# Performance work log

Hardware: AMD Instinct MI355X
Metric: run time of the kernel (lower is better)

Reference implementation:

```python
import jax, jax.numpy as jnp
import numpy as np

N_DF = 96      # number of deep-filtered frequency bins
BASE = 0       # base_bin
N_ORDER = 5    # FIR taps along time


def setup_inputs() -> dict:
    key = jax.random.key(0)
    k1, k2 = jax.random.split(key)
    B, T, F = 8, 3000, 481
    # complex spectrogram stored as [..., 2] = (real, imag)
    spec = jax.random.normal(k1, (B, T, F, 2), dtype=jnp.float32)
    # per-frame complex FIR coefficients: [..., :N_ORDER]=real, [..., N_ORDER:]=imag
    coef = jax.random.normal(k2, (B, T, N_DF, 2 * N_ORDER), dtype=jnp.float32)
    return {"spec": spec, "coef": coef}


def _df_forward(spec, coef):
    T = spec.shape[1]
    # narrow to the deep-filter band
    xr = spec[:, :, BASE:BASE + N_DF, 0]  # [B,T,N_DF]
    xi = spec[:, :, BASE:BASE + N_DF, 1]
    # causal pad along time (ConstantPad2d((0,0,n_order-1,0)))
    pad = ((0, 0), (N_ORDER - 1, 0), (0, 0))
    pr = jnp.pad(xr, pad)
    pi = jnp.pad(xi, pad)
    # unfold(time, n_order, 1) -> [B,T,N_DF,N_ORDER]; loop is over fixed tap count
    ur = jnp.stack([pr[:, k:k + T] for k in range(N_ORDER)], axis=-1)
    ui = jnp.stack([pi[:, k:k + T] for k in range(N_ORDER)], axis=-1)
    cr = coef[..., :N_ORDER]
    ci = coef[..., N_ORDER:]
    # complex sliding dot product: sum_k u[k] * c[k]
    fr = jnp.sum(ur * cr - ui * ci, axis=-1)  # [B,T,N_DF]
    fi = jnp.sum(ur * ci + ui * cr, axis=-1)
    out = spec.at[:, :, BASE:BASE + N_DF, 0].set(fr)
    out = out.at[:, :, BASE:BASE + N_DF, 1].set(fi)
    return out


def reference(spec, coef):
    return _df_forward(spec, coef)
```

## Files before the change

### kernel.cpp

```cpp
#include <hip/hip_runtime.h>


#define BN   8
#define TN   3000
#define FN   481
#define NDF  96
#define NORD 5

__global__ __launch_bounds__(256) void df_kernel(const float* __restrict__ spec,
                                                 const float* __restrict__ coef,
                                                 float* __restrict__ out) {
    const int i = blockIdx.x * blockDim.x + threadIdx.x;
    const int nFilt = BN * TN * NDF;
    const int nTot  = BN * TN * FN;
    if (i >= nTot) return;

    const int rowStride = FN * 2;

    if (i < nFilt) {
        const int f  = i % NDF;
        const int bt = i / NDF;
        const int t  = bt % TN;

        const float2* c2 = (const float2*)(coef + (size_t)i * (2 * NORD));
        const float2 ca = c2[0], cb = c2[1], cc = c2[2], cd = c2[3], ce = c2[4];
        const float cr[NORD] = {ca.x, ca.y, cb.x, cb.y, cc.x};
        const float ci[NORD] = {cc.y, cd.x, cd.y, ce.x, ce.y};

        const int base0 = bt * rowStride + f * 2;

        float fr = 0.f, fi = 0.f;
        if (t >= NORD - 1) {
            #pragma unroll
            for (int k = 0; k < NORD; ++k) {
                const float2 x = *(const float2*)(spec + base0 + (k - (NORD - 1)) * rowStride);
                fr += x.x * cr[k] - x.y * ci[k];
                fi += x.x * ci[k] + x.y * cr[k];
            }
        } else {
            #pragma unroll
            for (int k = 0; k < NORD; ++k) {
                const int tt = t - (NORD - 1) + k;
                if (tt >= 0) {
                    const float2 x = *(const float2*)(spec + base0 + (k - (NORD - 1)) * rowStride);
                    fr += x.x * cr[k] - x.y * ci[k];
                    fi += x.x * ci[k] + x.y * cr[k];
                }
            }
        }
        *(float2*)(out + base0) = make_float2(fr, fi);
    } else {
        const int j  = i - nFilt;
        const int f  = NDF + j % (FN - NDF);
        const int bt = j / (FN - NDF);
        const int idx = bt * rowStride + f * 2;
        *(float2*)(out + idx) = *(const float2*)(spec + idx);
    }
}

extern "C" void kernel_launch(void* const* d_in, const int* in_sizes, int n_in,
                              void* d_out, int out_size, void* d_ws, size_t ws_size,
                              hipStream_t stream) {
    const float* spec = (const float*)d_in[0];
    const float* coef = (const float*)d_in[1];
    float* out = (float*)d_out;

    const int nTot = BN * TN * FN;
    const int block = 256;
    const int grid = (nTot + block - 1) / block;
    df_kernel<<<grid, block, 0, stream>>>(spec, coef, out);
}
```

Before: 226.4 us.

## Stage coefficients via coalesced LDS loads and vectorize passthrough copy with float4

Filter blocks now load their contiguous 10-float coefficient slab with coalesced float4 loads into shared memory, replacing strided per-thread float2 reads. The copy region handles row alignment parity so most of each row moves as float4, plus one float2 per row, cutting the number of memory instructions and threads. The costs are added shared-memory traffic, a block barrier, and some index arithmetic.

```diff
diff --git a/kernel.cpp b/kernel.cpp
--- a/kernel.cpp
+++ b/kernel.cpp
@@ -6,55 +6,72 @@
 #define FN   481
 #define NDF  96
 #define NORD 5
+#define ROWF (FN * 2)
+#define NROWS (BN * TN)
+#define NFILT (NROWS * NDF)
+#define FILT_BLOCKS (NFILT / 256)
+#define COPYU 193
+#define NCOPY (NROWS * COPYU)
+#define COPY_BLOCKS ((NCOPY + 255) / 256)
 
-__global__ __launch_bounds__(256) void df_kernel(const float* __restrict__ spec,
-                                                 const float* __restrict__ coef,
-                                                 float* __restrict__ out) {
-    const int i = blockIdx.x * blockDim.x + threadIdx.x;
-    const int nFilt = BN * TN * NDF;
-    const int nTot  = BN * TN * FN;
-    if (i >= nTot) return;
+__global__ __launch_bounds__(256) void df_fused(const float* __restrict__ spec,
+                                                const float* __restrict__ coef,
+                                                float* __restrict__ out) {
+    const int blk = blockIdx.x;
+    const int tid = threadIdx.x;
 
-    const int rowStride = FN * 2;
+    if (blk < FILT_BLOCKS) {
+        __shared__ __align__(16) float cbuf[256 * 10];
+        {
+            const float4* src = (const float4*)(coef + (size_t)blk * 2560);
+            float4* dst = (float4*)cbuf;
+            dst[tid]       = src[tid];
+            dst[tid + 256] = src[tid + 256];
+            if (tid < 128) dst[tid + 512] = src[tid + 512];
+        }
+        __syncthreads();
 
-    if (i < nFilt) {
+        const int i  = blk * 256 + tid;
         const int f  = i % NDF;
         const int bt = i / NDF;
         const int t  = bt % TN;
-
-        const float2* c2 = (const float2*)(coef + (size_t)i * (2 * NORD));
-        const float2 ca = c2[0], cb = c2[1], cc = c2[2], cd = c2[3], ce = c2[4];
-        const float cr[NORD] = {ca.x, ca.y, cb.x, cb.y, cc.x};
-        const float ci[NORD] = {cc.y, cd.x, cd.y, ce.x, ce.y};
-
-        const int base0 = bt * rowStride + f * 2;
+        const float* my = cbuf + tid * 10;
+        const int base0 = bt * ROWF + f * 2;
 
         float fr = 0.f, fi = 0.f;
         if (t >= NORD - 1) {
             #pragma unroll
             for (int k = 0; k < NORD; ++k) {
-                const float2 x = *(const float2*)(spec + base0 + (k - (NORD - 1)) * rowStride);
-                fr += x.x * cr[k] - x.y * ci[k];
-                fi += x.x * ci[k] + x.y * cr[k];
+                const float2 x = *(const float2*)(spec + base0 + (k - 4) * ROWF);
+                fr += x.x * my[k]     - x.y * my[5 + k];
+                fi += x.x * my[5 + k] + x.y * my[k];
             }
         } else {
             #pragma unroll
             for (int k = 0; k < NORD; ++k) {
-                const int tt = t - (NORD - 1) + k;
+                const int tt = t - 4 + k;
                 if (tt >= 0) {
-                    const float2 x = *(const float2*)(spec + base0 + (k - (NORD - 1)) * rowStride);
-                    fr += x.x * cr[k] - x.y * ci[k];
-                    fi += x.x * ci[k] + x.y * cr[k];
+                    const float2 x = *(const float2*)(spec + base0 + (k - 4) * ROWF);
+                    fr += x.x * my[k]     - x.y * my[5 + k];
+                    fi += x.x * my[5 + k] + x.y * my[k];
                 }
             }
         }
         *(float2*)(out + base0) = make_float2(fr, fi);
     } else {
-        const int j  = i - nFilt;
-        const int f  = NDF + j % (FN - NDF);
-        const int bt = j / (FN - NDF);
-        const int idx = bt * rowStride + f * 2;
-        *(float2*)(out + idx) = *(const float2*)(spec + idx);
+        const int j = (blk - FILT_BLOCKS) * 256 + tid;
+        if (j >= NCOPY) return;
+        const int r = j / COPYU;
+        const int u = j - r * COPYU;
+        const int rb = r * ROWF;
+        const bool evenRow = (r & 1) == 0;
+        if (u < 192) {
+            const int off = rb + (evenRow ? 192 : 194) + 4 * u;
+            *(float4*)(out + off) = *(const float4*)(spec + off);
+        } else {
+            const int off = rb + (evenRow ? 960 : 192);
+            *(float2*)(out + off) = *(const float2*)(spec + off);
+        }
     }
 }
 
@@ -65,8 +82,6 @@
     const float* coef = (const float*)d_in[1];
     float* out = (float*)d_out;
 
-    const int nTot = BN * TN * FN;
-    const int block = 256;
-    const int grid = (nTot + block - 1) / block;
-    df_kernel<<<grid, block, 0, stream>>>(spec, coef, out);
+    const int grid = FILT_BLOCKS + COPY_BLOCKS;
+    df_fused<<<grid, 256, 0, stream>>>(spec, coef, out);
 }
```

Measured after the change: 231.4 us. 2.2% more time.

## Split into vectorized full copy plus two-frame-per-thread deep filter kernel

Applied to the files above, without the earlier changes.

Replaces the single mixed kernel with two launches. The first does a float4 copy of the whole spectrogram with 8 loads in flight per thread. The second computes two consecutive time frames per thread, sharing the overlapping 6-sample window to cut redundant spec loads. The filtered band is now written twice: once by the copy and again by the filter, which adds some traffic and a second launch.

```diff
diff --git a/kernel.cpp b/kernel.cpp
--- a/kernel.cpp
+++ b/kernel.cpp
@@ -5,57 +5,88 @@
 #define TN   3000
 #define FN   481
 #define NDF  96
-#define NORD 5
+#define ROWF (FN * 2)
+#define NROWS (BN * TN)
+#define NT4  ((NROWS * ROWF) / 4)
+#define CPB  2048
+#define COPY_GRID ((NT4 + CPB - 1) / CPB)
+#define TPAIRS (TN / 2)
+#define NFILT_T (BN * TPAIRS * NDF)
+#define FILT_GRID (NFILT_T / 256)
 
-__global__ __launch_bounds__(256) void df_kernel(const float* __restrict__ spec,
+__global__ __launch_bounds__(256) void copy_all(const float4* __restrict__ src,
+                                                float4* __restrict__ dst) {
+    const int base = blockIdx.x * CPB + threadIdx.x;
+    if (blockIdx.x < COPY_GRID - 1) {
+        float4 v[8];
+        #pragma unroll
+        for (int k = 0; k < 8; ++k) v[k] = src[base + k * 256];
+        #pragma unroll
+        for (int k = 0; k < 8; ++k) dst[base + k * 256] = v[k];
+    } else {
+        float4 v[8];
+        #pragma unroll
+        for (int k = 0; k < 8; ++k) {
+            const int idx = base + k * 256;
+            if (idx < NT4) v[k] = src[idx];
+        }
+        #pragma unroll
+        for (int k = 0; k < 8; ++k) {
+            const int idx = base + k * 256;
+            if (idx < NT4) dst[idx] = v[k];
+        }
+    }
+}
+
+__global__ __launch_bounds__(256) void df_filter(const float* __restrict__ spec,
                                                  const float* __restrict__ coef,
                                                  float* __restrict__ out) {
-    const int i = blockIdx.x * blockDim.x + threadIdx.x;
-    const int nFilt = BN * TN * NDF;
-    const int nTot  = BN * TN * FN;
-    if (i >= nTot) return;
+    const int i  = blockIdx.x * 256 + threadIdx.x;
+    const int f  = i % NDF;
+    const int r  = i / NDF;
+    const int tp = r % TPAIRS;
+    const int b  = r / TPAIRS;
+    const int t0 = tp * 2;
 
-    const int rowStride = FN * 2;
+    const int row0 = (b * TN + t0) * ROWF + f * 2;
+    const float* sp = spec + row0;
 
-    if (i < nFilt) {
-        const int f  = i % NDF;
-        const int bt = i / NDF;
-        const int t  = bt % TN;
+    float2 xs[6];
+    if (t0 >= 4) {
+        #pragma unroll
+        for (int j = 0; j < 6; ++j)
+            xs[j] = *(const float2*)(sp + (j - 4) * ROWF);
+    } else {
+        #pragma unroll
+        for (int j = 0; j < 6; ++j) {
+            const int tt = t0 - 4 + j;
+            xs[j] = (tt >= 0) ? *(const float2*)(sp + (j - 4) * ROWF)
+                              : make_float2(0.f, 0.f);
+        }
+    }
 
-        const float2* c2 = (const float2*)(coef + (size_t)i * (2 * NORD));
-        const float2 ca = c2[0], cb = c2[1], cc = c2[2], cd = c2[3], ce = c2[4];
-        const float cr[NORD] = {ca.x, ca.y, cb.x, cb.y, cc.x};
-        const float ci[NORD] = {cc.y, cd.x, cd.y, ce.x, ce.y};
+    const float2* c0 = (const float2*)(coef + (size_t)((b * TN + t0) * NDF + f) * 10);
+    const float2* c1 = c0 + NDF * 5;
+    const float2 a0 = c0[0], a1 = c0[1], a2 = c0[2], a3 = c0[3], a4 = c0[4];
+    const float2 b0 = c1[0], b1 = c1[1], b2 = c1[2], b3 = c1[3], b4 = c1[4];
+    const float cr0[5] = {a0.x, a0.y, a1.x, a1.y, a2.x};
+    const float ci0[5] = {a2.y, a3.x, a3.y, a4.x, a4.y};
+    const float cr1[5] = {b0.x, b0.y, b1.x, b1.y, b2.x};
+    const float ci1[5] = {b2.y, b3.x, b3.y, b4.x, b4.y};
 
-        const int base0 = bt * rowStride + f * 2;
+    float fr0 = 0.f, fi0 = 0.f, fr1 = 0.f, fi1 = 0.f;
+    #pragma unroll
+    for (int k = 0; k < 5; ++k) {
+        const float2 x0 = xs[k];
+        fr0 += x0.x * cr0[k] - x0.y * ci0[k];
+        fi0 += x0.x * ci0[k] + x0.y * cr0[k];
+        const float2 x1 = xs[k + 1];
+        fr1 += x1.x * cr1[k] - x1.y * ci1[k];
+        fi1 += x1.x * ci1[k] + x1.y * cr1[k];
+    }
 
-        float fr = 0.f, fi = 0.f;
-        if (t >= NORD - 1) {
-            #pragma unroll
-            for (int k = 0; k < NORD; ++k) {
-                const float2 x = *(const float2*)(spec + base0 + (k - (NORD - 1)) * rowStride);
-                fr += x.x * cr[k] - x.y * ci[k];
-                fi += x.x * ci[k] + x.y * cr[k];
-            }
-        } else {
-            #pragma unroll
-            for (int k = 0; k < NORD; ++k) {
-                const int tt = t - (NORD - 1) + k;
-                if (tt >= 0) {
-                    const float2 x = *(const float2*)(spec + base0 + (k - (NORD - 1)) * rowStride);
-                    fr += x.x * cr[k] - x.y * ci[k];
-                    fi += x.x * ci[k] + x.y * cr[k];
-                }
-            }
-        }
-        *(float2*)(out + base0) = make_float2(fr, fi);
-    } else {
-        const int j  = i - nFilt;
-        const int f  = NDF + j % (FN - NDF);
-        const int bt = j / (FN - NDF);
-        const int idx = bt * rowStride + f * 2;
-        *(float2*)(out + idx) = *(const float2*)(spec + idx);
-    }
+    *(float2*)(out + row0)        = make_float2(fr0, fi0);
+    *(float2*)(out + row0 + ROWF) = make_float2(fr1, fi1);
 }
 
 extern "C" void kernel_launch(void* const* d_in, const int* in_sizes, int n_in,
@@ -65,8 +96,6 @@
     const float* coef = (const float*)d_in[1];
     float* out = (float*)d_out;
 
-    const int nTot = BN * TN * FN;
-    const int block = 256;
-    const int grid = (nTot + block - 1) / block;
-    df_kernel<<<grid, block, 0, stream>>>(spec, coef, out);
+    copy_all<<<COPY_GRID, 256, 0, stream>>>((const float4*)spec, (float4*)out);
+    df_filter<<<FILT_GRID, 256, 0, stream>>>(spec, coef, out);
 }
```

Result: no change. 227.0 us (+0.3%).
